# Kernel optimization log

Hardware: AMD Instinct MI355X
Metric: run time of the kernel (lower is better)

## Reference

```python
import jax, jax.numpy as jnp
import numpy as np

BN_EPS = 1e-5
SCI_NOTATION_THRESHOLD = 1e16  # python float repr uses 'e+' only for |v| >= 1e16
NEG_SLOPE = 0.5


def _rescale(x):
    # Mirrors: str(max_abs.item()).split('e+') -> divide by 10**exponent when repr is scientific.
    m = jnp.max(jnp.abs(x))
    exp = jnp.floor(jnp.log10(jnp.maximum(m, 1.0)))
    return jnp.where(m >= SCI_NOTATION_THRESHOLD, x / (10.0 ** exp), x)


def _block(x, w, b, g, beta):
    # Linear (+ rescale), BatchNorm1d training-mode (+ rescale), LeakyReLU(0.5) (+ rescale)
    x = _rescale(x @ w.T + b)
    mu = jnp.mean(x, axis=0)
    var = jnp.mean(jnp.square(x - mu), axis=0)  # biased var, as torch BN normalization
    x = _rescale(g * (x - mu) * jax.lax.rsqrt(var + BN_EPS) + beta)
    x = _rescale(jnp.where(x >= 0, x, NEG_SLOPE * x))
    return x


def _uniform(k, shape, fan_in):
    bound = 1.0 / np.sqrt(fan_in)
    return jax.random.uniform(k, shape, jnp.float32, -bound, bound)


def setup_inputs() -> dict:
    key = jax.random.key(0)
    ks = jax.random.split(key, 9)
    B, D = 32768, 512
    H1, H2, H3, O = 2048, 2048, 1024, 1
    return {
        "x": jax.random.normal(ks[0], (B, D), jnp.float32),
        "w1": _uniform(ks[1], (H1, D), D),
        "b1": _uniform(ks[2], (H1,), D),
        "g1": jnp.ones((H1,), jnp.float32),
        "be1": jnp.zeros((H1,), jnp.float32),
        "w2": _uniform(ks[3], (H2, H1), H1),
        "b2": _uniform(ks[4], (H2,), H1),
        "g2": jnp.ones((H2,), jnp.float32),
        "be2": jnp.zeros((H2,), jnp.float32),
        "w3": _uniform(ks[5], (H3, H2), H2),
        "b3": _uniform(ks[6], (H3,), H2),
        "g3": jnp.ones((H3,), jnp.float32),
        "be3": jnp.zeros((H3,), jnp.float32),
        "wout": _uniform(ks[7], (O, H3), H3),
        "bout": _uniform(ks[8], (O,), H3),
    }


def reference(x, w1, b1, g1, be1, w2, b2, g2, be2, w3, b3, g3, be3, wout, bout):
    x = _block(x, w1, b1, g1, be1)
    x = _block(x, w2, b2, g2, be2)
    x = _block(x, w3, b3, g3, be3)
    return x @ wout.T + bout  # [B, 1]
```

## Files before the change

### kernel.cpp

```cpp
#include <hip/hip_runtime.h>

typedef __bf16 bf16x8 __attribute__((ext_vector_type(8)));
typedef float f32x4 __attribute__((ext_vector_type(4)));
typedef unsigned short us8 __attribute__((ext_vector_type(8)));

typedef __attribute__((address_space(3))) void lds_void_t;
typedef const __attribute__((address_space(1))) void gbl_void_t;

__device__ __forceinline__ unsigned short f2bf(float f) {
    unsigned u = __builtin_bit_cast(unsigned, f);
    u += 0x7FFFu + ((u >> 16) & 1u);
    return (unsigned short)(u >> 16);
}
__device__ __forceinline__ float bf2f(unsigned short h) {
    unsigned u = ((unsigned)h) << 16;
    return __builtin_bit_cast(float, u);
}

__global__ void report_ws(float* out, float v) { out[0] = v; }

__global__ __launch_bounds__(256) void cast_bf16(
    const float* __restrict__ src, unsigned short* __restrict__ dst, size_t n8)
{
    size_t i = (size_t)blockIdx.x * 256 + threadIdx.x;
    if (i >= n8) return;
    const float4* s = (const float4*)src + i * 2;
    float4 a = s[0], b = s[1];
    us8 o;
    o[0] = f2bf(a.x); o[1] = f2bf(a.y); o[2] = f2bf(a.z); o[3] = f2bf(a.w);
    o[4] = f2bf(b.x); o[5] = f2bf(b.y); o[6] = f2bf(b.z); o[7] = f2bf(b.w);
    *((us8*)dst + i) = o;
}


#define LOAD_AQ(QH) \
  _Pragma("unroll") for (int mm = 0; mm < 4; ++mm) \
    _Pragma("unroll") for (int s = 0; s < 2; ++s) \
      aq[mm][s] = *(const bf16x8*)&lds[aoff + ((QH)*64 + mm*16 + fr)*64 + (((s*4 + fq) ^ w7) << 3)];

#define LOAD_BP(G) \
  _Pragma("unroll") for (int nn = 0; nn < 2; ++nn) \
    _Pragma("unroll") for (int s = 0; s < 2; ++s) \
      bq[(G)*2+nn][s] = *(const bf16x8*)&lds[boff + ((wc&1)*64 + ((G)*2+nn)*16 + fr)*64 + (((s*4 + fq) ^ w7) << 3)];

#define MFMA_QUAD(QH, G) \
  _Pragma("unroll") for (int mm = 0; mm < 4; ++mm) \
    _Pragma("unroll") for (int nn = 0; nn < 2; ++nn) \
      _Pragma("unroll") for (int s = 0; s < 2; ++s) \
        acc[(QH)*4+mm][(G)*2+nn] = __builtin_amdgcn_mfma_f32_16x16x32_bf16( \
            aq[mm][s], bq[(G)*2+nn][s], acc[(QH)*4+mm][(G)*2+nn], 0, 0, 0);

__global__ __launch_bounds__(512, 2) void gemm256(
    const unsigned short* __restrict__ A,
    const unsigned short* __restrict__ W,
    const float* __restrict__ bias,
    unsigned short* __restrict__ Y,
    float* __restrict__ psum, float* __restrict__ psumsq,
    int M, int N, int K, int rowBlkBase)
{
    __shared__ unsigned short lds[65536];

    const int nbx = N >> 8;
    const int nwg = gridDim.x;
    const int cpx = nwg >> 3;
    const int bid = blockIdx.x;
    const int swzb = (bid & 7) * cpx + (bid >> 3);
    const int bm = swzb / nbx;
    const int bn = swzb % nbx;

    const int t    = threadIdx.x;
    const int wid  = t >> 6;
    const int lane = t & 63;
    const int wrh  = wid >> 2;
    const int wc   = wid & 3;
    const int fr   = lane & 15;
    const int fq   = lane >> 4;
    const int w7   = fr & 7;

    const int r0s  = t >> 3;
    const int ce   = (((t & 7) ^ ((t >> 3) & 7)) << 3);

    const size_t baseA = (size_t)(bm << 8) * K;
    const size_t baseW = (size_t)(bn << 8) * K;
    const int NT = K >> 6;

    auto STAGE = [&](int b, int op, int h, int kt) {
        const unsigned short* gsrc = (op ? W : A)
            + (op ? baseW : baseA)
            + (size_t)((h << 7) + r0s) * K + (kt << 6) + ce;
        char* dst = (char*)lds + ((((b * 2 + op) * 2 + h) << 14) + (wid << 10));
        __builtin_amdgcn_global_load_lds((gbl_void_t*)gsrc, (lds_void_t*)dst, 16, 0, 0);
        __builtin_amdgcn_global_load_lds((gbl_void_t*)(gsrc + (size_t)64 * K),
                                         (lds_void_t*)(dst + 8192), 16, 0, 0);
    };

    f32x4 acc[8][4];
#pragma unroll
    for (int m = 0; m < 8; ++m)
#pragma unroll
        for (int n = 0; n < 4; ++n)
            acc[m][n] = (f32x4){0.f, 0.f, 0.f, 0.f};

    STAGE(0, 1, 0, 0); STAGE(0, 1, 1, 0);
    STAGE(0, 0, 0, 0); STAGE(0, 0, 1, 0);
    if (NT > 1) { STAGE(1, 1, 0, 1); STAGE(1, 1, 1, 1); }
    asm volatile("s_waitcnt vmcnt(4)" ::: "memory");
    __builtin_amdgcn_s_barrier();

    bf16x8 aq[4][2], bq[4][2];

    for (int kt = 0; kt < NT; ++kt) {
        const int b = kt & 1;
        const unsigned aoff = (unsigned)(b * 4 + wrh) * 8192;
        const unsigned boff = (unsigned)(b * 4 + 2 + (wc >> 1)) * 8192;

        LOAD_AQ(0);
        LOAD_BP(0);
        if (kt + 1 < NT) STAGE(b ^ 1, 0, 0, kt + 1);
        __builtin_amdgcn_s_barrier();
        asm volatile("s_waitcnt lgkmcnt(0)" ::: "memory");
        __builtin_amdgcn_s_setprio(1);
        MFMA_QUAD(0, 0);
        __builtin_amdgcn_s_setprio(0);
        __builtin_amdgcn_s_barrier();

        LOAD_BP(1);
        if (kt + 1 < NT) STAGE(b ^ 1, 0, 1, kt + 1);
        __builtin_amdgcn_s_barrier();
        asm volatile("s_waitcnt lgkmcnt(0)" ::: "memory");
        __builtin_amdgcn_s_setprio(1);
        MFMA_QUAD(0, 1);
        __builtin_amdgcn_s_setprio(0);
        __builtin_amdgcn_s_barrier();

        LOAD_AQ(1);
        if (kt + 2 < NT) STAGE(b, 1, 0, kt + 2);
        __builtin_amdgcn_s_barrier();
        asm volatile("s_waitcnt lgkmcnt(0)" ::: "memory");
        __builtin_amdgcn_s_setprio(1);
        MFMA_QUAD(1, 0);
        __builtin_amdgcn_s_setprio(0);
        __builtin_amdgcn_s_barrier();

        if (kt + 2 < NT) {
            STAGE(b, 1, 1, kt + 2);
            asm volatile("s_waitcnt vmcnt(4)" ::: "memory");
        } else {
            asm volatile("s_waitcnt vmcnt(0)" ::: "memory");
        }
        __builtin_amdgcn_s_barrier();
        __builtin_amdgcn_s_setprio(1);
        MFMA_QUAD(1, 1);
        __builtin_amdgcn_s_setprio(0);
        __builtin_amdgcn_s_barrier();
    }

    float bv[4];
#pragma unroll
    for (int nn = 0; nn < 4; ++nn) bv[nn] = bias[(bn << 8) + wc * 64 + nn * 16 + fr];

    float* sSum = (float*)lds;
    float* sSq  = (float*)lds + 256 * 8;
#pragma unroll
    for (int nn = 0; nn < 4; ++nn) {
        float s = 0.f, q = 0.f;
#pragma unroll
        for (int mm = 0; mm < 8; ++mm)
#pragma unroll
            for (int r = 0; r < 4; ++r) {
                float v = acc[mm][nn][r] + bv[nn];
                s += v; q += v * v;
            }
        const int col = wc * 64 + nn * 16 + fr;
        const int sl  = wrh * 4 + fq;
        sSum[col * 8 + sl] = s;
        sSq [col * 8 + sl] = q;
    }
    __syncthreads();
    if (t < 256) {
        float s = 0.f, q = 0.f;
#pragma unroll
        for (int k = 0; k < 8; ++k) { s += sSum[t * 8 + k]; q += sSq[t * 8 + k]; }
        psum  [(size_t)(rowBlkBase + bm) * N + (bn << 8) + t] = s;
        psumsq[(size_t)(rowBlkBase + bm) * N + (bn << 8) + t] = q;
    }
    __syncthreads();

#pragma unroll
    for (int nn = 0; nn < 4; ++nn) {
        const int col = wc * 64 + nn * 16 + fr;
#pragma unroll
        for (int mm = 0; mm < 8; ++mm) {
            const int row0 = wrh * 128 + mm * 16 + fq * 4;
#pragma unroll
            for (int r = 0; r < 4; ++r)
                lds[(row0 + r) * 256 + col] = f2bf(acc[mm][nn][r] + bv[nn]);
        }
    }
    __syncthreads();

    {
        const size_t outBase = (size_t)(bm << 8) * N + (bn << 8);
#pragma unroll
        for (int i = 0; i < 16; ++i) {
            const int u   = t + i * 512;
            const int row = u >> 5, sl = u & 31;
            us8 v = *(const us8*)&lds[row * 256 + sl * 8];
            *(us8*)&Y[outBase + (size_t)row * N + sl * 8] = v;
        }
    }
}

__global__ __launch_bounds__(256) void col_stats2(
    const float* __restrict__ psum, const float* __restrict__ psumsq,
    const float* __restrict__ g, const float* __restrict__ be,
    float* __restrict__ scale, float* __restrict__ shift,
    int N, int NB, float invM)
{
    const int col = blockIdx.x * 256 + threadIdx.x;
    float s = 0.f, ss = 0.f;
    for (int c = 0; c < NB; ++c) {
        s  += psum  [(size_t)c * N + col];
        ss += psumsq[(size_t)c * N + col];
    }
    float mu  = s * invM;
    float var = ss * invM - mu * mu;
    float a = g[col] * rsqrtf(var + 1e-5f);
    scale[col] = a;
    shift[col] = be[col] - mu * a;
}

__global__ __launch_bounds__(256) void norm_copy(
    const unsigned short* __restrict__ src, unsigned short* __restrict__ dst,
    const float* __restrict__ scale, const float* __restrict__ shift,
    unsigned colMask8, size_t n8)
{
    size_t i = (size_t)blockIdx.x * 256 + threadIdx.x;
    if (i >= n8) return;
    us8 v = *((const us8*)src + i);
    const unsigned c8 = (unsigned)i & colMask8;
    const float4* sc = (const float4*)scale + c8 * 2;
    const float4* sh = (const float4*)shift + c8 * 2;
    float4 s0 = sc[0], s1 = sc[1], h0 = sh[0], h1 = sh[1];
    float xs[8];
    xs[0] = bf2f(v[0]) * s0.x + h0.x;  xs[1] = bf2f(v[1]) * s0.y + h0.y;
    xs[2] = bf2f(v[2]) * s0.z + h0.z;  xs[3] = bf2f(v[3]) * s0.w + h0.w;
    xs[4] = bf2f(v[4]) * s1.x + h1.x;  xs[5] = bf2f(v[5]) * s1.y + h1.y;
    xs[6] = bf2f(v[6]) * s1.z + h1.z;  xs[7] = bf2f(v[7]) * s1.w + h1.w;
    us8 o;
#pragma unroll
    for (int j = 0; j < 8; ++j) {
        float x = xs[j];
        x = (x >= 0.f) ? x : 0.5f * x;
        o[j] = f2bf(x);
    }
    *((us8*)dst + i) = o;
}

__global__ __launch_bounds__(256) void matvec_norm_out(
    const unsigned short* __restrict__ X, const float* __restrict__ scale,
    const float* __restrict__ shift, const float* __restrict__ wvec,
    const float* __restrict__ bout, float* __restrict__ out, int Kd)
{
    const int row  = blockIdx.x * 4 + (threadIdx.x >> 6);
    const int lane = threadIdx.x & 63;
    const unsigned short* xr = X + (size_t)row * Kd;
    float s = 0.f;
    for (int j = lane * 8; j < Kd; j += 512) {
        us8 x = *(const us8*)(xr + j);
        const float4* sc = (const float4*)(scale + j);
        const float4* sh = (const float4*)(shift + j);
        const float4* wv = (const float4*)(wvec + j);
        float4 s0 = sc[0], s1 = sc[1], h0 = sh[0], h1 = sh[1];
        float4 w0 = wv[0], w1 = wv[1];
        float xs[8] = {
            bf2f(x[0]) * s0.x + h0.x, bf2f(x[1]) * s0.y + h0.y,
            bf2f(x[2]) * s0.z + h0.z, bf2f(x[3]) * s0.w + h0.w,
            bf2f(x[4]) * s1.x + h1.x, bf2f(x[5]) * s1.y + h1.y,
            bf2f(x[6]) * s1.z + h1.z, bf2f(x[7]) * s1.w + h1.w };
        float wf[8] = { w0.x, w0.y, w0.z, w0.w, w1.x, w1.y, w1.z, w1.w };
#pragma unroll
        for (int e = 0; e < 8; ++e) {
            float xv = xs[e];
            xv = (xv >= 0.f) ? xv : 0.5f * xv;
            s += xv * wf[e];
        }
    }
#pragma unroll
    for (int off = 32; off > 0; off >>= 1) s += __shfl_down(s, off);
    if (lane == 0) out[row] = s + bout[0];
}

extern "C" void kernel_launch(void* const* d_in, const int* in_sizes, int n_in,
                              void* d_out, int out_size, void* d_ws, size_t ws_size,
                              hipStream_t stream)
{
    const float* x    = (const float*)d_in[0];
    const float* w1   = (const float*)d_in[1];
    const float* b1   = (const float*)d_in[2];
    const float* g1   = (const float*)d_in[3];
    const float* be1  = (const float*)d_in[4];
    const float* w2   = (const float*)d_in[5];
    const float* b2   = (const float*)d_in[6];
    const float* g2   = (const float*)d_in[7];
    const float* be2  = (const float*)d_in[8];
    const float* w3   = (const float*)d_in[9];
    const float* b3   = (const float*)d_in[10];
    const float* g3   = (const float*)d_in[11];
    const float* be3  = (const float*)d_in[12];
    const float* wout = (const float*)d_in[13];
    const float* bout = (const float*)d_in[14];
    float* out = (float*)d_out;

    const int B = 32768, D = 512, H1 = 2048, H2 = 2048, H3 = 1024;
    const int NB = B / 256;
    const int RCH = 8192;

    char* ws = (char*)d_ws;
    size_t off = 0;
    auto alloc = [&](size_t bytes) -> char* {
        char* p = ws + off;
        off += (bytes + 255) & ~(size_t)255;
        return p;
    };
    unsigned short* bufA    = (unsigned short*)alloc((size_t)B * H1 * 2);
    unsigned short* scratch = (unsigned short*)alloc((size_t)RCH * H1 * 2);
    unsigned short* W1b     = (unsigned short*)alloc((size_t)H1 * D * 2);
    unsigned short* W2b     = (unsigned short*)alloc((size_t)H2 * H1 * 2);
    unsigned short* W3b     = (unsigned short*)alloc((size_t)H3 * H2 * 2);
    float* psum   = (float*)alloc((size_t)NB * H1 * 4);
    float* psumsq = (float*)alloc((size_t)NB * H1 * 4);
    float* scale  = (float*)alloc((size_t)H1 * 4);
    float* shift  = (float*)alloc((size_t)H1 * 4);

    if (off > ws_size) {
        report_ws<<<1, 1, 0, stream>>>(out, (float)ws_size);
        return;
    }

    {
        size_t n8;
        n8 = (size_t)B * D / 8;   cast_bf16<<<(unsigned)((n8 + 255) / 256), 256, 0, stream>>>(x,  scratch, n8);
        n8 = (size_t)H1 * D / 8;  cast_bf16<<<(unsigned)((n8 + 255) / 256), 256, 0, stream>>>(w1, W1b, n8);
        n8 = (size_t)H2 * H1 / 8; cast_bf16<<<(unsigned)((n8 + 255) / 256), 256, 0, stream>>>(w2, W2b, n8);
        n8 = (size_t)H3 * H2 / 8; cast_bf16<<<(unsigned)((n8 + 255) / 256), 256, 0, stream>>>(w3, W3b, n8);
    }

    const float invB = 1.0f / (float)B;
    const size_t chunk8 = (size_t)RCH * H1 / 8;

    gemm256<<<(B / 256) * (H1 / 256), 512, 0, stream>>>(
        scratch, W1b, b1, bufA, psum, psumsq, B, H1, D, 0);
    col_stats2<<<H1 / 256, 256, 0, stream>>>(psum, psumsq, g1, be1, scale, shift, H1, NB, invB);

    for (int c = 0; c < B / RCH; ++c) {
        norm_copy<<<(unsigned)(chunk8 / 256), 256, 0, stream>>>(
            bufA + (size_t)c * RCH * H1, scratch, scale, shift, H1 / 8 - 1, chunk8);
        gemm256<<<(RCH / 256) * (H2 / 256), 512, 0, stream>>>(
            scratch, W2b, b2, bufA + (size_t)c * RCH * H1, psum, psumsq,
            RCH, H2, H1, c * (RCH / 256));
    }
    col_stats2<<<H2 / 256, 256, 0, stream>>>(psum, psumsq, g2, be2, scale, shift, H2, NB, invB);

    for (int c = 0; c < B / RCH; ++c) {
        norm_copy<<<(unsigned)(chunk8 / 256), 256, 0, stream>>>(
            bufA + (size_t)c * RCH * H2, scratch, scale, shift, H2 / 8 - 1, chunk8);
        gemm256<<<(RCH / 256) * (H3 / 256), 512, 0, stream>>>(
            scratch, W3b, b3, bufA + (size_t)c * RCH * H3, psum, psumsq,
            RCH, H3, H2, c * (RCH / 256));
    }
    col_stats2<<<H3 / 256, 256, 0, stream>>>(psum, psumsq, g3, be3, scale, shift, H3, NB, invB);

    matvec_norm_out<<<B / 4, 256, 0, stream>>>(bufA, scale, shift, wout, bout, out, H3);
}
```

Measured before the change: 803.6 us.

## Use full-batch ping-pong buffers instead of row-chunked GEMM passes when workspace allows

When the workspace can hold two full B×H1 bf16 buffers, each layer now runs as one full-batch GEMM plus one full normalize pass, with the bf16 input and W1 placed inside the second buffer. This removes the four-chunk norm/GEMM launch sequence and its smaller grids, which underfill the device. The normalize kernel becomes grid-stride with a fixed 2048-block grid, LeakyReLU is written as fmaxf(x, 0.5x), and a partial lgkmcnt wait is added before the first barrier in the GEMM loop. The chunked path is kept as a fallback, at the cost of needing roughly twice the workspace.

```diff
diff --git a/kernel.cpp b/kernel.cpp
--- a/kernel.cpp
+++ b/kernel.cpp
@@ -117,6 +117,7 @@
         LOAD_AQ(0);
         LOAD_BP(0);
         if (kt + 1 < NT) STAGE(b ^ 1, 0, 0, kt + 1);
+        asm volatile("s_waitcnt lgkmcnt(8)" ::: "memory");
         __builtin_amdgcn_s_barrier();
         asm volatile("s_waitcnt lgkmcnt(0)" ::: "memory");
         __builtin_amdgcn_s_setprio(1);
@@ -230,31 +231,32 @@
     shift[col] = be[col] - mu * a;
 }
 
-__global__ __launch_bounds__(256) void norm_copy(
+__global__ __launch_bounds__(256) void norm_full(
     const unsigned short* __restrict__ src, unsigned short* __restrict__ dst,
     const float* __restrict__ scale, const float* __restrict__ shift,
     unsigned colMask8, size_t n8)
 {
-    size_t i = (size_t)blockIdx.x * 256 + threadIdx.x;
-    if (i >= n8) return;
-    us8 v = *((const us8*)src + i);
-    const unsigned c8 = (unsigned)i & colMask8;
-    const float4* sc = (const float4*)scale + c8 * 2;
-    const float4* sh = (const float4*)shift + c8 * 2;
-    float4 s0 = sc[0], s1 = sc[1], h0 = sh[0], h1 = sh[1];
-    float xs[8];
-    xs[0] = bf2f(v[0]) * s0.x + h0.x;  xs[1] = bf2f(v[1]) * s0.y + h0.y;
-    xs[2] = bf2f(v[2]) * s0.z + h0.z;  xs[3] = bf2f(v[3]) * s0.w + h0.w;
-    xs[4] = bf2f(v[4]) * s1.x + h1.x;  xs[5] = bf2f(v[5]) * s1.y + h1.y;
-    xs[6] = bf2f(v[6]) * s1.z + h1.z;  xs[7] = bf2f(v[7]) * s1.w + h1.w;
-    us8 o;
-#pragma unroll
-    for (int j = 0; j < 8; ++j) {
-        float x = xs[j];
-        x = (x >= 0.f) ? x : 0.5f * x;
-        o[j] = f2bf(x);
-    }
-    *((us8*)dst + i) = o;
+    const size_t stride = (size_t)gridDim.x * 256;
+    for (size_t i = (size_t)blockIdx.x * 256 + threadIdx.x; i < n8; i += stride) {
+        us8 v = *((const us8*)src + i);
+        const unsigned c8 = (unsigned)i & colMask8;
+        const float4* sc = (const float4*)scale + c8 * 2;
+        const float4* sh = (const float4*)shift + c8 * 2;
+        float4 s0 = sc[0], s1 = sc[1], h0 = sh[0], h1 = sh[1];
+        float xs[8];
+        xs[0] = bf2f(v[0]) * s0.x + h0.x;  xs[1] = bf2f(v[1]) * s0.y + h0.y;
+        xs[2] = bf2f(v[2]) * s0.z + h0.z;  xs[3] = bf2f(v[3]) * s0.w + h0.w;
+        xs[4] = bf2f(v[4]) * s1.x + h1.x;  xs[5] = bf2f(v[5]) * s1.y + h1.y;
+        xs[6] = bf2f(v[6]) * s1.z + h1.z;  xs[7] = bf2f(v[7]) * s1.w + h1.w;
+        us8 o;
+#pragma unroll
+        for (int j = 0; j < 8; ++j) {
+            float x = xs[j];
+            x = fmaxf(x, 0.5f * x);
+            o[j] = f2bf(x);
+        }
+        *((us8*)dst + i) = o;
+    }
 }
 
 __global__ __launch_bounds__(256) void matvec_norm_out(
@@ -282,7 +284,7 @@
 #pragma unroll
         for (int e = 0; e < 8; ++e) {
             float xv = xs[e];
-            xv = (xv >= 0.f) ? xv : 0.5f * xv;
+            xv = fmaxf(xv, 0.5f * xv);
             s += xv * wf[e];
         }
     }
@@ -314,62 +316,106 @@
 
     const int B = 32768, D = 512, H1 = 2048, H2 = 2048, H3 = 1024;
     const int NB = B / 256;
-    const int RCH = 8192;
-
+    const float invB = 1.0f / (float)B;
     char* ws = (char*)d_ws;
-    size_t off = 0;
-    auto alloc = [&](size_t bytes) -> char* {
-        char* p = ws + off;
-        off += (bytes + 255) & ~(size_t)255;
-        return p;
-    };
-    unsigned short* bufA    = (unsigned short*)alloc((size_t)B * H1 * 2);
-    unsigned short* scratch = (unsigned short*)alloc((size_t)RCH * H1 * 2);
-    unsigned short* W1b     = (unsigned short*)alloc((size_t)H1 * D * 2);
-    unsigned short* W2b     = (unsigned short*)alloc((size_t)H2 * H1 * 2);
-    unsigned short* W3b     = (unsigned short*)alloc((size_t)H3 * H2 * 2);
-    float* psum   = (float*)alloc((size_t)NB * H1 * 4);
-    float* psumsq = (float*)alloc((size_t)NB * H1 * 4);
-    float* scale  = (float*)alloc((size_t)H1 * 4);
-    float* shift  = (float*)alloc((size_t)H1 * 4);
-
-    if (off > ws_size) {
-        report_ws<<<1, 1, 0, stream>>>(out, (float)ws_size);
-        return;
-    }
 
     {
+        size_t off = 0;
+        auto alloc = [&](size_t bytes) -> char* {
+            char* p = ws + off;
+            off += (bytes + 255) & ~(size_t)255;
+            return p;
+        };
+        unsigned short* bufA = (unsigned short*)alloc((size_t)B * H1 * 2);
+        unsigned short* bufB = (unsigned short*)alloc((size_t)B * H1 * 2);
+        unsigned short* W2b  = (unsigned short*)alloc((size_t)H2 * H1 * 2);
+        unsigned short* W3b  = (unsigned short*)alloc((size_t)H3 * H2 * 2);
+        float* psum   = (float*)alloc((size_t)NB * H1 * 4);
+        float* psumsq = (float*)alloc((size_t)NB * H1 * 4);
+        float* scale  = (float*)alloc((size_t)H1 * 4);
+        float* shift  = (float*)alloc((size_t)H1 * 4);
+        unsigned short* W1b = bufB;
+        unsigned short* Xb  = bufB + ((size_t)B * H1 - (size_t)B * D);
+
+        if (off <= ws_size) {
+            size_t n8;
+            n8 = (size_t)B * D / 8;   cast_bf16<<<(unsigned)((n8 + 255) / 256), 256, 0, stream>>>(x,  Xb,  n8);
+            n8 = (size_t)H1 * D / 8;  cast_bf16<<<(unsigned)((n8 + 255) / 256), 256, 0, stream>>>(w1, W1b, n8);
+            n8 = (size_t)H2 * H1 / 8; cast_bf16<<<(unsigned)((n8 + 255) / 256), 256, 0, stream>>>(w2, W2b, n8);
+            n8 = (size_t)H3 * H2 / 8; cast_bf16<<<(unsigned)((n8 + 255) / 256), 256, 0, stream>>>(w3, W3b, n8);
+
+            gemm256<<<(B / 256) * (H1 / 256), 512, 0, stream>>>(
+                Xb, W1b, b1, bufA, psum, psumsq, B, H1, D, 0);
+            col_stats2<<<H1 / 256, 256, 0, stream>>>(psum, psumsq, g1, be1, scale, shift, H1, NB, invB);
+            norm_full<<<2048, 256, 0, stream>>>(bufA, bufB, scale, shift, H1 / 8 - 1, (size_t)B * H1 / 8);
+
+            gemm256<<<(B / 256) * (H2 / 256), 512, 0, stream>>>(
+                bufB, W2b, b2, bufA, psum, psumsq, B, H2, H1, 0);
+            col_stats2<<<H2 / 256, 256, 0, stream>>>(psum, psumsq, g2, be2, scale, shift, H2, NB, invB);
+            norm_full<<<2048, 256, 0, stream>>>(bufA, bufB, scale, shift, H2 / 8 - 1, (size_t)B * H2 / 8);
+
+            gemm256<<<(B / 256) * (H3 / 256), 512, 0, stream>>>(
+                bufB, W3b, b3, bufA, psum, psumsq, B, H3, H2, 0);
+            col_stats2<<<H3 / 256, 256, 0, stream>>>(psum, psumsq, g3, be3, scale, shift, H3, NB, invB);
+
+            matvec_norm_out<<<B / 4, 256, 0, stream>>>(bufA, scale, shift, wout, bout, out, H3);
+            return;
+        }
+    }
+
+    {
+        const int RCH = 8192;
+        size_t off = 0;
+        auto alloc = [&](size_t bytes) -> char* {
+            char* p = ws + off;
+            off += (bytes + 255) & ~(size_t)255;
+            return p;
+        };
+        unsigned short* bufA    = (unsigned short*)alloc((size_t)B * H1 * 2);
+        unsigned short* scratch = (unsigned short*)alloc((size_t)RCH * H1 * 2);
+        unsigned short* W1b     = (unsigned short*)alloc((size_t)H1 * D * 2);
+        unsigned short* W2b     = (unsigned short*)alloc((size_t)H2 * H1 * 2);
+        unsigned short* W3b     = (unsigned short*)alloc((size_t)H3 * H2 * 2);
+        float* psum   = (float*)alloc((size_t)NB * H1 * 4);
+        float* psumsq = (float*)alloc((size_t)NB * H1 * 4);
+        float* scale  = (float*)alloc((size_t)H1 * 4);
+        float* shift  = (float*)alloc((size_t)H1 * 4);
+
+        if (off > ws_size) {
+            report_ws<<<1, 1, 0, stream>>>(out, (float)ws_size);
+            return;
+        }
+
         size_t n8;
         n8 = (size_t)B * D / 8;   cast_bf16<<<(unsigned)((n8 + 255) / 256), 256, 0, stream>>>(x,  scratch, n8);
         n8 = (size_t)H1 * D / 8;  cast_bf16<<<(unsigned)((n8 + 255) / 256), 256, 0, stream>>>(w1, W1b, n8);
         n8 = (size_t)H2 * H1 / 8; cast_bf16<<<(unsigned)((n8 + 255) / 256), 256, 0, stream>>>(w2, W2b, n8);
         n8 = (size_t)H3 * H2 / 8; cast_bf16<<<(unsigned)((n8 + 255) / 256), 256, 0, stream>>>(w3, W3b, n8);
-    }
-
-    const float invB = 1.0f / (float)B;
-    const size_t chunk8 = (size_t)RCH * H1 / 8;
-
-    gemm256<<<(B / 256) * (H1 / 256), 512, 0, stream>>>(
-        scratch, W1b, b1, bufA, psum, psumsq, B, H1, D, 0);
-    col_stats2<<<H1 / 256, 256, 0, stream>>>(psum, psumsq, g1, be1, scale, shift, H1, NB, invB);
-
-    for (int c = 0; c < B / RCH; ++c) {
-        norm_copy<<<(unsigned)(chunk8 / 256), 256, 0, stream>>>(
-            bufA + (size_t)c * RCH * H1, scratch, scale, shift, H1 / 8 - 1, chunk8);
-        gemm256<<<(RCH / 256) * (H2 / 256), 512, 0, stream>>>(
-            scratch, W2b, b2, bufA + (size_t)c * RCH * H1, psum, psumsq,
-            RCH, H2, H1, c * (RCH / 256));
-    }
-    col_stats2<<<H2 / 256, 256, 0, stream>>>(psum, psumsq, g2, be2, scale, shift, H2, NB, invB);
-
-    for (int c = 0; c < B / RCH; ++c) {
-        norm_copy<<<(unsigned)(chunk8 / 256), 256, 0, stream>>>(
-            bufA + (size_t)c * RCH * H2, scratch, scale, shift, H2 / 8 - 1, chunk8);
-        gemm256<<<(RCH / 256) * (H3 / 256), 512, 0, stream>>>(
-            scratch, W3b, b3, bufA + (size_t)c * RCH * H3, psum, psumsq,
-            RCH, H3, H2, c * (RCH / 256));
-    }
-    col_stats2<<<H3 / 256, 256, 0, stream>>>(psum, psumsq, g3, be3, scale, shift, H3, NB, invB);
-
-    matvec_norm_out<<<B / 4, 256, 0, stream>>>(bufA, scale, shift, wout, bout, out, H3);
-}
+
+        const size_t chunk8 = (size_t)RCH * H1 / 8;
+
+        gemm256<<<(B / 256) * (H1 / 256), 512, 0, stream>>>(
+            scratch, W1b, b1, bufA, psum, psumsq, B, H1, D, 0);
+        col_stats2<<<H1 / 256, 256, 0, stream>>>(psum, psumsq, g1, be1, scale, shift, H1, NB, invB);
+
+        for (int c = 0; c < B / RCH; ++c) {
+            norm_full<<<2048, 256, 0, stream>>>(
+                bufA + (size_t)c * RCH * H1, scratch, scale, shift, H1 / 8 - 1, chunk8);
+            gemm256<<<(RCH / 256) * (H2 / 256), 512, 0, stream>>>(
+                scratch, W2b, b2, bufA + (size_t)c * RCH * H1, psum, psumsq,
+                RCH, H2, H1, c * (RCH / 256));
+        }
+        col_stats2<<<H2 / 256, 256, 0, stream>>>(psum, psumsq, g2, be2, scale, shift, H2, NB, invB);
+
+        for (int c = 0; c < B / RCH; ++c) {
+            norm_full<<<2048, 256, 0, stream>>>(
+                bufA + (size_t)c * RCH * H2, scratch, scale, shift, H2 / 8 - 1, chunk8);
+            gemm256<<<(RCH / 256) * (H3 / 256), 512, 0, stream>>>(
+                scratch, W3b, b3, bufA + (size_t)c * RCH * H3, psum, psumsq,
+                RCH, H3, H2, c * (RCH / 256));
+        }
+        col_stats2<<<H3 / 256, 256, 0, stream>>>(psum, psumsq, g3, be3, scale, shift, H3, NB, invB);
+
+        matvec_norm_out<<<B / 4, 256, 0, stream>>>(bufA, scale, shift, wout, bout, out, H3);
+    }
+}
```

After: 802.2 us. About the same (-0.2%).

## Fuse BN+LeakyReLU into layer-3 GEMM A-load and enlarge layer-2 chunks

Applied to the files above, without the earlier changes.

Adds a templated GEMM variant that loads raw layer-2 outputs through registers, applies BN scale/shift and LeakyReLU, and writes the bf16 result into LDS. Layer 3 no longer needs separate normalize-copy passes. Layer 2 uses 16384-row chunks with a grid-stride normalize kernel, and layer 3 writes to a separate buffer. This removes the round trip of the normalized layer-3 input through global memory and cuts launch count. In exchange, A loads no longer go directly from global memory to LDS, and the per-tile VALU transform must overlap with the MFMAs.

```diff
diff --git a/kernel.cpp b/kernel.cpp
--- a/kernel.cpp
+++ b/kernel.cpp
@@ -50,15 +50,18 @@
         acc[(QH)*4+mm][(G)*2+nn] = __builtin_amdgcn_mfma_f32_16x16x32_bf16( \
             aq[mm][s], bq[(G)*2+nn][s], acc[(QH)*4+mm][(G)*2+nn], 0, 0, 0);
 
+template<bool NORMA>
 __global__ __launch_bounds__(512, 2) void gemm256(
     const unsigned short* __restrict__ A,
     const unsigned short* __restrict__ W,
     const float* __restrict__ bias,
     unsigned short* __restrict__ Y,
     float* __restrict__ psum, float* __restrict__ psumsq,
-    int M, int N, int K, int rowBlkBase)
+    int M, int N, int K, int rowBlkBase,
+    const float* __restrict__ nsc, const float* __restrict__ nsh)
 {
     __shared__ unsigned short lds[65536];
+    __shared__ float ntab[4096];
 
     const int nbx = N >> 8;
     const int nwg = gridDim.x;
@@ -94,6 +97,37 @@
                                          (lds_void_t*)(dst + 8192), 16, 0, 0);
     };
 
+    us8 av[4];
+    auto ALOAD = [&](int kt) {
+        const unsigned short* a0 = A + baseA + (size_t)(kt << 6) + ce;
+        av[0] = *(const us8*)(a0 + (size_t)(r0s)       * K);
+        av[1] = *(const us8*)(a0 + (size_t)(r0s + 64)  * K);
+        av[2] = *(const us8*)(a0 + (size_t)(r0s + 128) * K);
+        av[3] = *(const us8*)(a0 + (size_t)(r0s + 192) * K);
+    };
+    auto XFORM = [&](int bdst, int kt) {
+        const int cb = (kt << 6) + ce;
+        float4 s0 = *(const float4*)&ntab[cb];
+        float4 s1 = *(const float4*)&ntab[cb + 4];
+        float4 h0 = *(const float4*)&ntab[2048 + cb];
+        float4 h1 = *(const float4*)&ntab[2048 + cb + 4];
+        float scv[8] = {s0.x,s0.y,s0.z,s0.w,s1.x,s1.y,s1.z,s1.w};
+        float shv[8] = {h0.x,h0.y,h0.z,h0.w,h1.x,h1.y,h1.z,h1.w};
+#pragma unroll
+        for (int q = 0; q < 4; ++q) {
+            us8 o;
+#pragma unroll
+            for (int e = 0; e < 8; ++e) {
+                float f = bf2f(av[q][e]);
+                float y = f * scv[e] + shv[e];
+                y = fmaxf(y, 0.5f * y);
+                o[e] = f2bf(y);
+            }
+            const int h = q >> 1, l = q & 1;
+            *(us8*)&lds[((unsigned)(bdst * 4 + h) << 13) + l * 4096 + t * 8] = o;
+        }
+    };
+
     f32x4 acc[8][4];
 #pragma unroll
     for (int m = 0; m < 8; ++m)
@@ -101,10 +135,21 @@
         for (int n = 0; n < 4; ++n)
             acc[m][n] = (f32x4){0.f, 0.f, 0.f, 0.f};
 
+    if constexpr (NORMA) {
+        ((float4*)ntab)[t]       = ((const float4*)nsc)[t];
+        ((float4*)ntab)[512 + t] = ((const float4*)nsh)[t];
+    }
     STAGE(0, 1, 0, 0); STAGE(0, 1, 1, 0);
-    STAGE(0, 0, 0, 0); STAGE(0, 0, 1, 0);
+    if constexpr (!NORMA) { STAGE(0, 0, 0, 0); STAGE(0, 0, 1, 0); }
+    else                  { ALOAD(0); }
     if (NT > 1) { STAGE(1, 1, 0, 1); STAGE(1, 1, 1, 1); }
-    asm volatile("s_waitcnt vmcnt(4)" ::: "memory");
+    if constexpr (NORMA) {
+        __syncthreads();
+        XFORM(0, 0);
+        asm volatile("s_waitcnt lgkmcnt(0)" ::: "memory");
+    } else {
+        asm volatile("s_waitcnt vmcnt(4)" ::: "memory");
+    }
     __builtin_amdgcn_s_barrier();
 
     bf16x8 aq[4][2], bq[4][2];
@@ -116,7 +161,11 @@
 
         LOAD_AQ(0);
         LOAD_BP(0);
-        if (kt + 1 < NT) STAGE(b ^ 1, 0, 0, kt + 1);
+        if (kt + 1 < NT) {
+            if constexpr (NORMA) { ALOAD(kt + 1); __builtin_amdgcn_sched_barrier(0); }
+            else                 { STAGE(b ^ 1, 0, 0, kt + 1); }
+        }
+        asm volatile("s_waitcnt lgkmcnt(8)" ::: "memory");
         __builtin_amdgcn_s_barrier();
         asm volatile("s_waitcnt lgkmcnt(0)" ::: "memory");
         __builtin_amdgcn_s_setprio(1);
@@ -125,7 +174,7 @@
         __builtin_amdgcn_s_barrier();
 
         LOAD_BP(1);
-        if (kt + 1 < NT) STAGE(b ^ 1, 0, 1, kt + 1);
+        if constexpr (!NORMA) { if (kt + 1 < NT) STAGE(b ^ 1, 0, 1, kt + 1); }
         __builtin_amdgcn_s_barrier();
         asm volatile("s_waitcnt lgkmcnt(0)" ::: "memory");
         __builtin_amdgcn_s_setprio(1);
@@ -142,17 +191,23 @@
         __builtin_amdgcn_s_setprio(0);
         __builtin_amdgcn_s_barrier();
 
-        if (kt + 2 < NT) {
-            STAGE(b, 1, 1, kt + 2);
-            asm volatile("s_waitcnt vmcnt(4)" ::: "memory");
+        if (kt + 2 < NT) STAGE(b, 1, 1, kt + 2);
+        if constexpr (NORMA) {
+            __builtin_amdgcn_s_setprio(1);
+            MFMA_QUAD(1, 1);
+            __builtin_amdgcn_s_setprio(0);
+            if (kt + 1 < NT) XFORM(b ^ 1, kt + 1);
+            asm volatile("s_waitcnt lgkmcnt(0)" ::: "memory");
+            __builtin_amdgcn_s_barrier();
         } else {
-            asm volatile("s_waitcnt vmcnt(0)" ::: "memory");
-        }
-        __builtin_amdgcn_s_barrier();
-        __builtin_amdgcn_s_setprio(1);
-        MFMA_QUAD(1, 1);
-        __builtin_amdgcn_s_setprio(0);
-        __builtin_amdgcn_s_barrier();
+            if (kt + 2 < NT) { asm volatile("s_waitcnt vmcnt(4)" ::: "memory"); }
+            else             { asm volatile("s_waitcnt vmcnt(0)" ::: "memory"); }
+            __builtin_amdgcn_s_barrier();
+            __builtin_amdgcn_s_setprio(1);
+            MFMA_QUAD(1, 1);
+            __builtin_amdgcn_s_setprio(0);
+            __builtin_amdgcn_s_barrier();
+        }
     }
 
     float bv[4];
@@ -198,7 +253,6 @@
         }
     }
     __syncthreads();
-
     {
         const size_t outBase = (size_t)(bm << 8) * N + (bn << 8);
 #pragma unroll
@@ -230,31 +284,32 @@
     shift[col] = be[col] - mu * a;
 }
 
-__global__ __launch_bounds__(256) void norm_copy(
+__global__ __launch_bounds__(256) void norm_full(
     const unsigned short* __restrict__ src, unsigned short* __restrict__ dst,
     const float* __restrict__ scale, const float* __restrict__ shift,
     unsigned colMask8, size_t n8)
 {
-    size_t i = (size_t)blockIdx.x * 256 + threadIdx.x;
-    if (i >= n8) return;
-    us8 v = *((const us8*)src + i);
-    const unsigned c8 = (unsigned)i & colMask8;
-    const float4* sc = (const float4*)scale + c8 * 2;
-    const float4* sh = (const float4*)shift + c8 * 2;
-    float4 s0 = sc[0], s1 = sc[1], h0 = sh[0], h1 = sh[1];
-    float xs[8];
-    xs[0] = bf2f(v[0]) * s0.x + h0.x;  xs[1] = bf2f(v[1]) * s0.y + h0.y;
-    xs[2] = bf2f(v[2]) * s0.z + h0.z;  xs[3] = bf2f(v[3]) * s0.w + h0.w;
-    xs[4] = bf2f(v[4]) * s1.x + h1.x;  xs[5] = bf2f(v[5]) * s1.y + h1.y;
-    xs[6] = bf2f(v[6]) * s1.z + h1.z;  xs[7] = bf2f(v[7]) * s1.w + h1.w;
-    us8 o;
-#pragma unroll
-    for (int j = 0; j < 8; ++j) {
-        float x = xs[j];
-        x = (x >= 0.f) ? x : 0.5f * x;
-        o[j] = f2bf(x);
-    }
-    *((us8*)dst + i) = o;
+    const size_t stride = (size_t)gridDim.x * 256;
+    for (size_t i = (size_t)blockIdx.x * 256 + threadIdx.x; i < n8; i += stride) {
+        us8 v = *((const us8*)src + i);
+        const unsigned c8 = (unsigned)i & colMask8;
+        const float4* sc = (const float4*)scale + c8 * 2;
+        const float4* sh = (const float4*)shift + c8 * 2;
+        float4 s0 = sc[0], s1 = sc[1], h0 = sh[0], h1 = sh[1];
+        float xs[8];
+        xs[0] = bf2f(v[0]) * s0.x + h0.x;  xs[1] = bf2f(v[1]) * s0.y + h0.y;
+        xs[2] = bf2f(v[2]) * s0.z + h0.z;  xs[3] = bf2f(v[3]) * s0.w + h0.w;
+        xs[4] = bf2f(v[4]) * s1.x + h1.x;  xs[5] = bf2f(v[5]) * s1.y + h1.y;
+        xs[6] = bf2f(v[6]) * s1.z + h1.z;  xs[7] = bf2f(v[7]) * s1.w + h1.w;
+        us8 o;
+#pragma unroll
+        for (int j = 0; j < 8; ++j) {
+            float x = xs[j];
+            x = fmaxf(x, 0.5f * x);
+            o[j] = f2bf(x);
+        }
+        *((us8*)dst + i) = o;
+    }
 }
 
 __global__ __launch_bounds__(256) void matvec_norm_out(
@@ -282,7 +337,7 @@
 #pragma unroll
         for (int e = 0; e < 8; ++e) {
             float xv = xs[e];
-            xv = (xv >= 0.f) ? xv : 0.5f * xv;
+            xv = fmaxf(xv, 0.5f * xv);
             s += xv * wf[e];
         }
     }
@@ -314,20 +369,21 @@
 
     const int B = 32768, D = 512, H1 = 2048, H2 = 2048, H3 = 1024;
     const int NB = B / 256;
-    const int RCH = 8192;
-
+    const int RCH = 16384;
+    const float invB = 1.0f / (float)B;
     char* ws = (char*)d_ws;
+
     size_t off = 0;
     auto alloc = [&](size_t bytes) -> char* {
         char* p = ws + off;
         off += (bytes + 255) & ~(size_t)255;
         return p;
     };
-    unsigned short* bufA    = (unsigned short*)alloc((size_t)B * H1 * 2);
-    unsigned short* scratch = (unsigned short*)alloc((size_t)RCH * H1 * 2);
-    unsigned short* W1b     = (unsigned short*)alloc((size_t)H1 * D * 2);
-    unsigned short* W2b     = (unsigned short*)alloc((size_t)H2 * H1 * 2);
-    unsigned short* W3b     = (unsigned short*)alloc((size_t)H3 * H2 * 2);
+    unsigned short* bufA  = (unsigned short*)alloc((size_t)B * H1 * 2);
+    unsigned short* bufY3 = (unsigned short*)alloc((size_t)B * H3 * 2);
+    unsigned short* W1b   = (unsigned short*)alloc((size_t)H1 * D * 2);
+    unsigned short* W2b   = (unsigned short*)alloc((size_t)H2 * H1 * 2);
+    unsigned short* W3b   = (unsigned short*)alloc((size_t)H3 * H2 * 2);
     float* psum   = (float*)alloc((size_t)NB * H1 * 4);
     float* psumsq = (float*)alloc((size_t)NB * H1 * 4);
     float* scale  = (float*)alloc((size_t)H1 * 4);
@@ -340,36 +396,29 @@
 
     {
         size_t n8;
-        n8 = (size_t)B * D / 8;   cast_bf16<<<(unsigned)((n8 + 255) / 256), 256, 0, stream>>>(x,  scratch, n8);
+        n8 = (size_t)B * D / 8;   cast_bf16<<<(unsigned)((n8 + 255) / 256), 256, 0, stream>>>(x,  bufY3, n8);
         n8 = (size_t)H1 * D / 8;  cast_bf16<<<(unsigned)((n8 + 255) / 256), 256, 0, stream>>>(w1, W1b, n8);
         n8 = (size_t)H2 * H1 / 8; cast_bf16<<<(unsigned)((n8 + 255) / 256), 256, 0, stream>>>(w2, W2b, n8);
         n8 = (size_t)H3 * H2 / 8; cast_bf16<<<(unsigned)((n8 + 255) / 256), 256, 0, stream>>>(w3, W3b, n8);
     }
 
-    const float invB = 1.0f / (float)B;
+    gemm256<false><<<(B / 256) * (H1 / 256), 512, 0, stream>>>(
+        bufY3, W1b, b1, bufA, psum, psumsq, B, H1, D, 0, nullptr, nullptr);
+    col_stats2<<<H1 / 256, 256, 0, stream>>>(psum, psumsq, g1, be1, scale, shift, H1, NB, invB);
+
     const size_t chunk8 = (size_t)RCH * H1 / 8;
-
-    gemm256<<<(B / 256) * (H1 / 256), 512, 0, stream>>>(
-        scratch, W1b, b1, bufA, psum, psumsq, B, H1, D, 0);
-    col_stats2<<<H1 / 256, 256, 0, stream>>>(psum, psumsq, g1, be1, scale, shift, H1, NB, invB);
-
     for (int c = 0; c < B / RCH; ++c) {
-        norm_copy<<<(unsigned)(chunk8 / 256), 256, 0, stream>>>(
-            bufA + (size_t)c * RCH * H1, scratch, scale, shift, H1 / 8 - 1, chunk8);
-        gemm256<<<(RCH / 256) * (H2 / 256), 512, 0, stream>>>(
-            scratch, W2b, b2, bufA + (size_t)c * RCH * H1, psum, psumsq,
-            RCH, H2, H1, c * (RCH / 256));
+        norm_full<<<2048, 256, 0, stream>>>(
+            bufA + (size_t)c * RCH * H1, bufY3, scale, shift, H1 / 8 - 1, chunk8);
+        gemm256<false><<<(RCH / 256) * (H2 / 256), 512, 0, stream>>>(
+            bufY3, W2b, b2, bufA + (size_t)c * RCH * H1, psum, psumsq,
+            RCH, H2, H1, c * (RCH / 256), nullptr, nullptr);
     }
     col_stats2<<<H2 / 256, 256, 0, stream>>>(psum, psumsq, g2, be2, scale, shift, H2, NB, invB);
 
-    for (int c = 0; c < B / RCH; ++c) {
-        norm_copy<<<(unsigned)(chunk8 / 256), 256, 0, stream>>>(
-            bufA + (size_t)c * RCH * H2, scratch, scale, shift, H2 / 8 - 1, chunk8);
-        gemm256<<<(RCH / 256) * (H3 / 256), 512, 0, stream>>>(
-            scratch, W3b, b3, bufA + (size_t)c * RCH * H3, psum, psumsq,
-            RCH, H3, H2, c * (RCH / 256));
-    }
+    gemm256<true><<<(B / 256) * (H3 / 256), 512, 0, stream>>>(
+        bufA, W3b, b3, bufY3, psum, psumsq, B, H3, H2, 0, scale, shift);
     col_stats2<<<H3 / 256, 256, 0, stream>>>(psum, psumsq, g3, be3, scale, shift, H3, NB, invB);
 
-    matvec_norm_out<<<B / 4, 256, 0, stream>>>(bufA, scale, shift, wout, bout, out, H3);
-}
+    matvec_norm_out<<<B / 4, 256, 0, stream>>>(bufY3, scale, shift, wout, bout, out, H3);
+}
```

After: 673.1 us. 16.2% less time.
